# Optimization experiments

Measured on AMD Instinct MI355X. Metric: run time of the kernel, lower is better.

Reference implementation:

```python
import jax, jax.numpy as jnp
import numpy as np
from jax import lax

T, H, W = 2048, 128, 160


def setup_inputs() -> dict:
    key = jax.random.key(0)
    k1, = jax.random.split(key, 1)
    batch_x = jax.random.uniform(k1, (T, 1, H, W), dtype=jnp.float32)
    # params = [close, open, dhot] / 255 (defaults 1, 5, 8)
    params = jnp.array([1.0, 5.0, 8.0], dtype=jnp.float32) / 255.0
    HT0 = jnp.zeros((H, W), dtype=jnp.float32)
    LT0 = jnp.zeros((H, W), dtype=jnp.float32)
    # ConvTranspose2d(1,1,3,padding=1) with constant weight ones/(3**2/2) = 2/9;
    # symmetric kernel + padding=1 transposed conv == SAME-padded standard conv.
    kernel = jnp.full((1, 1, 3, 3), 2.0 / 9.0, dtype=jnp.float32)
    return {"batch_x": batch_x, "params": params, "HT0": HT0, "LT0": LT0, "kernel": kernel}


def reference(batch_x, params, HT0, LT0, kernel):
    d_close, d_open, d_hot = params[0], params[1], params[2]

    def step(carry, x):
        HT, LT = carry
        img = x[0]  # (H, W)
        # hot scores computed against *pre-update* thresholds
        tmpH_hot = jax.nn.sigmoid((img - HT - d_hot) * 500.0)
        tmpH = (img - HT) > 0
        HT = jnp.where(tmpH, HT + d_open, HT - d_close)
        tmpL_hot = jax.nn.sigmoid((LT - img - d_hot) * 500.0)
        tmpL = (LT - img) > 0
        LT = jnp.where(tmpL, LT - d_open, LT + d_close)
        return (HT, LT), tmpH_hot + tmpL_hot

    _, hot = lax.scan(step, (HT0, LT0), batch_x)  # hot: (T, H, W)

    # DiffErosion: relu(1 - conv(1 - x)) with SAME padding, batched over frames
    where_zero = (1.0 - hot)[:, None, :, :]  # (T, 1, H, W)
    sub = lax.conv_general_dilated(
        where_zero, kernel, window_strides=(1, 1), padding="SAME",
        dimension_numbers=("NCHW", "OIHW", "NCHW"))
    return jax.nn.relu(1.0 - sub)  # (T, 1, H, W)
```

## Files before the change

kernel.cpp:

```cpp
#include <hip/hip_runtime.h>


#define TILE_W 16
#define TILE_H 16
#define IN_W 14
#define IN_H 14
#define BUF 16
#define PRE 32

constexpr int T_FRAMES = 2048;
constexpr int H_IMG = 128;
constexpr int W_IMG = 160;
constexpr int HW = H_IMG * W_IMG;
constexpr float C1 = 721.3475204444817f;

constexpr size_t ws_needed(int snap) {
    return (size_t)(T_FRAMES / snap - 1) * HW * sizeof(float2);
}

__device__ __forceinline__ float dpp_from_left(float v) {
    return __int_as_float(__builtin_amdgcn_update_dpp(0, __float_as_int(v), 0x111, 0xF, 0xF, true));
}
__device__ __forceinline__ float dpp_from_right(float v) {
    return __int_as_float(__builtin_amdgcn_update_dpp(0, __float_as_int(v), 0x101, 0xF, 0xF, true));
}

template <int SNAP_>
__global__ __launch_bounds__(256, 1)
void svs_scan(const float* __restrict__ x, const float* __restrict__ params,
              const float* __restrict__ HT0, const float* __restrict__ LT0,
              float2* __restrict__ snap)
{
    constexpr int TEFF_ = T_FRAMES - SNAP_;
    const int pix = (int)blockIdx.x * 256 + (int)threadIdx.x;
    const float dC = params[0];
    const float dO = params[1];

    float HT = HT0[pix];
    float LT = LT0[pix];
    const float* xp = x + pix;

    float va[PRE], vb[PRE];
    #pragma unroll
    for (int i = 0; i < PRE; ++i) va[i] = xp[i * HW];
    __builtin_amdgcn_sched_barrier(0);

    for (int t = 0; t < TEFF_; t += 2 * PRE) {
        #pragma unroll
        for (int i = 0; i < PRE; ++i) vb[i] = xp[(t + PRE + i) * HW];
        __builtin_amdgcn_sched_barrier(0);
        #pragma unroll
        for (int i = 0; i < PRE; ++i) {
            const float img = va[i];
            HT = ((img - HT) > 0.0f) ? (HT + dO) : (HT - dC);
            LT = ((LT - img) > 0.0f) ? (LT - dO) : (LT + dC);
        }
        if (((t + PRE) % SNAP_) == 0) {
            const int k = (t + PRE) / SNAP_ - 1;
            if (k >= 0 && k < T_FRAMES / SNAP_ - 1)
                snap[(size_t)k * HW + pix] = make_float2(HT, LT);
        }
        if (t + 2 * PRE < TEFF_) {
            #pragma unroll
            for (int i = 0; i < PRE; ++i) va[i] = xp[(t + 2 * PRE + i) * HW];
        }
        __builtin_amdgcn_sched_barrier(0);
        #pragma unroll
        for (int i = 0; i < PRE; ++i) {
            const float img = vb[i];
            HT = ((img - HT) > 0.0f) ? (HT + dO) : (HT - dC);
            LT = ((LT - img) > 0.0f) ? (LT - dO) : (LT + dC);
        }
        if (((t + 2 * PRE) % SNAP_) == 0) {
            const int k = (t + 2 * PRE) / SNAP_ - 1;
            if (k < T_FRAMES / SNAP_ - 1)
                snap[(size_t)k * HW + pix] = make_float2(HT, LT);
        }
    }
}

template <int SNAP_>
__global__ __launch_bounds__(256)
void svs_compute(const float* __restrict__ x, const float* __restrict__ params,
                 const float* __restrict__ HT0, const float* __restrict__ LT0,
                 const float* __restrict__ kern, const float2* __restrict__ snap,
                 float* __restrict__ out)
{
    constexpr int TOTAL_ = 120 * (T_FRAMES / SNAP_);
    const int lin = (int)blockIdx.x + 12 * (int)blockIdx.y + 120 * (int)blockIdx.z;
    const int w   = (lin & 7) * (TOTAL_ / 8) + (lin >> 3);
    const int bx  = w % 12;
    const int by  = (w / 12) % 10;
    const int slice = w / 120;

    const int tx = threadIdx.x & 15;
    const int ty = threadIdx.x >> 4;
    const int gx = bx * IN_W + tx - 1;
    const int gy = by * IN_H + ty - 1;
    const int t0 = slice * SNAP_;

    const bool valid = (gx >= 0) & (gx < W_IMG) & (gy >= 0) & (gy < H_IMG);
    const int cx = min(max(gx, 0), W_IMG - 1);
    const int cy = min(max(gy, 0), H_IMG - 1);
    const int pix = cy * W_IMG + cx;

    const float dC   = params[0];
    const float dO   = params[1];
    const float dHot = params[2];
    const float kw   = kern[4];
    const float c0   = dHot * C1;

    float HT, LT;
    if (slice == 0) {
        HT = valid ? HT0[pix] : 0.0f;
        LT = valid ? LT0[pix] : 0.0f;
    } else {
        const float2 s = snap[(size_t)(slice - 1) * HW + pix];
        HT = valid ? s.x : 0.0f;
        LT = valid ? s.y : 0.0f;
    }

    __shared__ float sm[TILE_H][BUF][TILE_W + 1];

    const bool doOut = (tx >= 1) & (tx <= IN_W) & (ty >= 1) & (ty <= IN_H) & valid;
    const int ym = max(ty - 1, 0);
    const int yp = min(ty + 1, TILE_H - 1);
    const float* xp = x + pix;
    float* op = out + pix;

    float v[BUF], vn[BUF], hot[BUF];
    #pragma unroll
    for (int i = 0; i < BUF; ++i) v[i] = xp[(t0 + i) * HW];

    for (int tb = t0; tb < t0 + SNAP_; tb += BUF) {
        const bool more = (tb + BUF) < (t0 + SNAP_);
        if (more) {
            #pragma unroll
            for (int i = 0; i < BUF; ++i) vn[i] = xp[(tb + BUF + i) * HW];
        }
        __builtin_amdgcn_sched_barrier(0);
        #pragma unroll
        for (int i = 0; i < BUF; ++i) {
            const float img = v[i];
            const float aH = img - HT;
            const float eH = __builtin_amdgcn_exp2f(fmaf(aH, -C1, c0));
            const float hH = __builtin_amdgcn_rcpf(1.0f + eH);
            HT = (aH > 0.0f) ? (HT + dO) : (HT - dC);
            const float aL = LT - img;
            const float eL = __builtin_amdgcn_exp2f(fmaf(aL, -C1, c0));
            const float hL = __builtin_amdgcn_rcpf(1.0f + eL);
            LT = (aL > 0.0f) ? (LT - dO) : (LT + dC);
            hot[i] = valid ? (hH + hL) : 1.0f;
            sm[ty][i][tx] = hot[i];
        }
        __syncthreads();
        #pragma unroll
        for (int i = 0; i < BUF; ++i) {
            const float r0 = sm[ym][i][tx];
            const float r1 = sm[yp][i][tx];
            const float vs = r0 + hot[i] + r1;
            const float S  = vs + dpp_from_left(vs) + dpp_from_right(vs);
            float o = fmaf(S, kw, -1.0f);
            o = fmaxf(o, 0.0f);
            if (doOut) op[(tb + i) * HW] = o;
        }
        __syncthreads();
        if (more) {
            #pragma unroll
            for (int i = 0; i < BUF; ++i) v[i] = vn[i];
        }
    }
}

extern "C" void kernel_launch(void* const* d_in, const int* in_sizes, int n_in,
                              void* d_out, int out_size, void* d_ws, size_t ws_size,
                              hipStream_t stream) {
    const float* x      = (const float*)d_in[0];
    const float* params = (const float*)d_in[1];
    const float* HT0p   = (const float*)d_in[2];
    const float* LT0p   = (const float*)d_in[3];
    const float* kern   = (const float*)d_in[4];
    float* out = (float*)d_out;

    if (ws_size >= ws_needed(64)) {
        float2* snap = (float2*)d_ws;
        svs_scan<64><<<dim3(HW / 256), dim3(256), 0, stream>>>(x, params, HT0p, LT0p, snap);
        svs_compute<64><<<dim3(12, 10, T_FRAMES / 64), dim3(256), 0, stream>>>(
            x, params, HT0p, LT0p, kern, snap, out);
    } else if (ws_size >= ws_needed(128)) {
        float2* snap = (float2*)d_ws;
        svs_scan<128><<<dim3(HW / 256), dim3(256), 0, stream>>>(x, params, HT0p, LT0p, snap);
        svs_compute<128><<<dim3(12, 10, T_FRAMES / 128), dim3(256), 0, stream>>>(
            x, params, HT0p, LT0p, kern, snap, out);
    } else {
        svs_compute<2048><<<dim3(12, 10, 1), dim3(256), 0, stream>>>(
            x, params, HT0p, LT0p, kern, (const float2*)d_ws, out);
    }
}
```

Baseline: 168.3 us.

## Retile compute kernel to 32x8 output tiles with split halo/output threads

Replaces the 16x16 tile (14x14 outputs with DPP horizontal sums) with a 34x10 haloed tile computed by 340 threads, while 256 threads read the 3x3 window from shared memory to produce a 32x8 output tile with full-width coalesced stores. This cuts the redundant halo recomputation of the sigmoid scan and makes stores 32-wide and aligned. In exchange it drops the register double-buffered prefetch of x, halves BUF to 8, removes the block-index swizzle, and leaves 44 threads idle.

```diff
diff --git a/kernel.cpp b/kernel.cpp
--- a/kernel.cpp
+++ b/kernel.cpp
@@ -1,11 +1,7 @@
 #include <hip/hip_runtime.h>
 
 
-#define TILE_W 16
-#define TILE_H 16
-#define IN_W 14
-#define IN_H 14
-#define BUF 16
+#define BUF 8
 #define PRE 32
 
 constexpr int T_FRAMES = 2048;
@@ -16,13 +12,6 @@
 
 constexpr size_t ws_needed(int snap) {
     return (size_t)(T_FRAMES / snap - 1) * HW * sizeof(float2);
-}
-
-__device__ __forceinline__ float dpp_from_left(float v) {
-    return __int_as_float(__builtin_amdgcn_update_dpp(0, __float_as_int(v), 0x111, 0xF, 0xF, true));
-}
-__device__ __forceinline__ float dpp_from_right(float v) {
-    return __int_as_float(__builtin_amdgcn_update_dpp(0, __float_as_int(v), 0x101, 0xF, 0xF, true));
 }
 
 template <int SNAP_>
@@ -80,29 +69,17 @@
 }
 
 template <int SNAP_>
-__global__ __launch_bounds__(256)
-void svs_compute(const float* __restrict__ x, const float* __restrict__ params,
-                 const float* __restrict__ HT0, const float* __restrict__ LT0,
-                 const float* __restrict__ kern, const float2* __restrict__ snap,
-                 float* __restrict__ out)
+__global__ __launch_bounds__(384)
+void svs_compute2(const float* __restrict__ x, const float* __restrict__ params,
+                  const float* __restrict__ HT0, const float* __restrict__ LT0,
+                  const float* __restrict__ kern, const float2* __restrict__ snap,
+                  float* __restrict__ out)
 {
-    constexpr int TOTAL_ = 120 * (T_FRAMES / SNAP_);
-    const int lin = (int)blockIdx.x + 12 * (int)blockIdx.y + 120 * (int)blockIdx.z;
-    const int w   = (lin & 7) * (TOTAL_ / 8) + (lin >> 3);
-    const int bx  = w % 12;
-    const int by  = (w / 12) % 10;
-    const int slice = w / 120;
-
-    const int tx = threadIdx.x & 15;
-    const int ty = threadIdx.x >> 4;
-    const int gx = bx * IN_W + tx - 1;
-    const int gy = by * IN_H + ty - 1;
+    const int tc = (int)blockIdx.x;
+    const int tr = (int)blockIdx.y;
+    const int slice = (int)blockIdx.z;
     const int t0 = slice * SNAP_;
-
-    const bool valid = (gx >= 0) & (gx < W_IMG) & (gy >= 0) & (gy < H_IMG);
-    const int cx = min(max(gx, 0), W_IMG - 1);
-    const int cy = min(max(gy, 0), H_IMG - 1);
-    const int pix = cy * W_IMG + cx;
+    const int t = (int)threadIdx.x;
 
     const float dC   = params[0];
     const float dO   = params[1];
@@ -110,65 +87,70 @@
     const float kw   = kern[4];
     const float c0   = dHot * C1;
 
-    float HT, LT;
-    if (slice == 0) {
-        HT = valid ? HT0[pix] : 0.0f;
-        LT = valid ? LT0[pix] : 0.0f;
-    } else {
-        const float2 s = snap[(size_t)(slice - 1) * HW + pix];
-        HT = valid ? s.x : 0.0f;
-        LT = valid ? s.y : 0.0f;
+    const bool tA = (t < 340);
+    const int  ca = tA ? (t % 34) : 0;
+    const int  lr = tA ? (t / 34) : 0;
+    const int  gcol = tc * 32 + ca - 1;
+    const int  grow = tr * 8 + lr - 1;
+    const bool valid = tA & (gcol >= 0) & (gcol < W_IMG) & (grow >= 0) & (grow < H_IMG);
+    const int  pix = min(max(grow, 0), H_IMG - 1) * W_IMG + min(max(gcol, 0), W_IMG - 1);
+    const float* xp = x + pix;
+
+    float HT = 0.0f, LT = 0.0f;
+    if (tA) {
+        if (slice == 0) {
+            HT = valid ? HT0[pix] : 0.0f;
+            LT = valid ? LT0[pix] : 0.0f;
+        } else {
+            const float2 s = snap[(size_t)(slice - 1) * HW + pix];
+            HT = valid ? s.x : 0.0f;
+            LT = valid ? s.y : 0.0f;
+        }
     }
 
-    __shared__ float sm[TILE_H][BUF][TILE_W + 1];
+    const bool tB = (t < 256);
+    const int  oc = t & 31;
+    const int  orow = t >> 5;
+    float* op = out + (size_t)(tr * 8 + orow) * W_IMG + (tc * 32 + oc);
 
-    const bool doOut = (tx >= 1) & (tx <= IN_W) & (ty >= 1) & (ty <= IN_H) & valid;
-    const int ym = max(ty - 1, 0);
-    const int yp = min(ty + 1, TILE_H - 1);
-    const float* xp = x + pix;
-    float* op = out + pix;
-
-    float v[BUF], vn[BUF], hot[BUF];
-    #pragma unroll
-    for (int i = 0; i < BUF; ++i) v[i] = xp[(t0 + i) * HW];
+    __shared__ float sm[10][BUF][36];
 
     for (int tb = t0; tb < t0 + SNAP_; tb += BUF) {
-        const bool more = (tb + BUF) < (t0 + SNAP_);
-        if (more) {
+        float v[BUF];
+        if (tA) {
             #pragma unroll
-            for (int i = 0; i < BUF; ++i) vn[i] = xp[(tb + BUF + i) * HW];
+            for (int i = 0; i < BUF; ++i) v[i] = xp[(tb + i) * HW];
         }
         __builtin_amdgcn_sched_barrier(0);
-        #pragma unroll
-        for (int i = 0; i < BUF; ++i) {
-            const float img = v[i];
-            const float aH = img - HT;
-            const float eH = __builtin_amdgcn_exp2f(fmaf(aH, -C1, c0));
-            const float hH = __builtin_amdgcn_rcpf(1.0f + eH);
-            HT = (aH > 0.0f) ? (HT + dO) : (HT - dC);
-            const float aL = LT - img;
-            const float eL = __builtin_amdgcn_exp2f(fmaf(aL, -C1, c0));
-            const float hL = __builtin_amdgcn_rcpf(1.0f + eL);
-            LT = (aL > 0.0f) ? (LT - dO) : (LT + dC);
-            hot[i] = valid ? (hH + hL) : 1.0f;
-            sm[ty][i][tx] = hot[i];
+        if (tA) {
+            #pragma unroll
+            for (int i = 0; i < BUF; ++i) {
+                const float img = v[i];
+                const float aH = img - HT;
+                const float eH = __builtin_amdgcn_exp2f(fmaf(aH, -C1, c0));
+                const float hH = __builtin_amdgcn_rcpf(1.0f + eH);
+                HT = (aH > 0.0f) ? (HT + dO) : (HT - dC);
+                const float aL = LT - img;
+                const float eL = __builtin_amdgcn_exp2f(fmaf(aL, -C1, c0));
+                const float hL = __builtin_amdgcn_rcpf(1.0f + eL);
+                LT = (aL > 0.0f) ? (LT - dO) : (LT + dC);
+                sm[lr][i][ca] = valid ? (hH + hL) : 1.0f;
+            }
         }
         __syncthreads();
-        #pragma unroll
-        for (int i = 0; i < BUF; ++i) {
-            const float r0 = sm[ym][i][tx];
-            const float r1 = sm[yp][i][tx];
-            const float vs = r0 + hot[i] + r1;
-            const float S  = vs + dpp_from_left(vs) + dpp_from_right(vs);
-            float o = fmaf(S, kw, -1.0f);
-            o = fmaxf(o, 0.0f);
-            if (doOut) op[(tb + i) * HW] = o;
+        if (tB) {
+            #pragma unroll
+            for (int i = 0; i < BUF; ++i) {
+                const float cs0 = sm[orow][i][oc    ] + sm[orow + 1][i][oc    ] + sm[orow + 2][i][oc    ];
+                const float cs1 = sm[orow][i][oc + 1] + sm[orow + 1][i][oc + 1] + sm[orow + 2][i][oc + 1];
+                const float cs2 = sm[orow][i][oc + 2] + sm[orow + 1][i][oc + 2] + sm[orow + 2][i][oc + 2];
+                const float S = cs0 + cs1 + cs2;
+                float o = fmaf(S, kw, -1.0f);
+                o = fmaxf(o, 0.0f);
+                op[(size_t)(tb + i) * HW] = o;
+            }
         }
         __syncthreads();
-        if (more) {
-            #pragma unroll
-            for (int i = 0; i < BUF; ++i) v[i] = vn[i];
-        }
     }
 }
 
@@ -185,15 +167,15 @@
     if (ws_size >= ws_needed(64)) {
         float2* snap = (float2*)d_ws;
         svs_scan<64><<<dim3(HW / 256), dim3(256), 0, stream>>>(x, params, HT0p, LT0p, snap);
-        svs_compute<64><<<dim3(12, 10, T_FRAMES / 64), dim3(256), 0, stream>>>(
+        svs_compute2<64><<<dim3(5, 16, T_FRAMES / 64), dim3(384), 0, stream>>>(
             x, params, HT0p, LT0p, kern, snap, out);
     } else if (ws_size >= ws_needed(128)) {
         float2* snap = (float2*)d_ws;
         svs_scan<128><<<dim3(HW / 256), dim3(256), 0, stream>>>(x, params, HT0p, LT0p, snap);
-        svs_compute<128><<<dim3(12, 10, T_FRAMES / 128), dim3(256), 0, stream>>>(
+        svs_compute2<128><<<dim3(5, 16, T_FRAMES / 128), dim3(384), 0, stream>>>(
             x, params, HT0p, LT0p, kern, snap, out);
     } else {
-        svs_compute<2048><<<dim3(12, 10, 1), dim3(256), 0, stream>>>(
+        svs_compute2<2048><<<dim3(5, 16, 1), dim3(384), 0, stream>>>(
             x, params, HT0p, LT0p, kern, (const float2*)d_ws, out);
     }
 }
```

Measured after the change: 170.7 us. About the same (+1.4%).

## Stream scan inputs through a deep LDS ring via global_load_lds

Applied to the files above, without the earlier changes.

Replaces the register-double-buffered scan with a single-wave-per-block kernel that keeps a 63-deep ring of frames in LDS. Loads are issued asynchronously with global_load_lds and throttled by explicit vmcnt waits. Each serial step issues one new load, so many loads stay in flight per lane and memory latency is hidden without large register arrays. It also removes the register prefetch from the compute kernel. The risks are 64-thread blocks giving lower occupancy per CU and per-frame waitcnt overhead on the serial recurrence; the old scan is kept only for the smaller-workspace path.

```diff
diff --git a/kernel.cpp b/kernel.cpp
--- a/kernel.cpp
+++ b/kernel.cpp
@@ -7,6 +7,7 @@
 #define IN_H 14
 #define BUF 16
 #define PRE 32
+#define DEPTH 63
 
 constexpr int T_FRAMES = 2048;
 constexpr int H_IMG = 128;
@@ -25,14 +26,26 @@
     return __int_as_float(__builtin_amdgcn_update_dpp(0, __float_as_int(v), 0x101, 0xF, 0xF, true));
 }
 
+#define WAITCNT_VM(N) __builtin_amdgcn_s_waitcnt((((N) & 0xF) | (((N) >> 4) << 14) | (0x7 << 4) | (0xF << 8)))
+#define SB0() __builtin_amdgcn_sched_barrier(0)
+
+typedef const unsigned int __attribute__((address_space(1)))* gas_ptr;
+typedef unsigned int __attribute__((address_space(3)))* las_ptr;
+#define GLLDS(g, l)                                                          \
+    __builtin_amdgcn_global_load_lds(                                        \
+        (gas_ptr)(unsigned long long)(g),                                    \
+        (las_ptr)(unsigned)(unsigned long long)(l), 4, 0, 0)
+
 template <int SNAP_>
-__global__ __launch_bounds__(256, 1)
-void svs_scan(const float* __restrict__ x, const float* __restrict__ params,
-              const float* __restrict__ HT0, const float* __restrict__ LT0,
-              float2* __restrict__ snap)
+__global__ __launch_bounds__(64, 1)
+void svs_scan_lds(const float* __restrict__ x, const float* __restrict__ params,
+                  const float* __restrict__ HT0, const float* __restrict__ LT0,
+                  float2* __restrict__ snap)
 {
     constexpr int TEFF_ = T_FRAMES - SNAP_;
-    const int pix = (int)blockIdx.x * 256 + (int)threadIdx.x;
+    constexpr int NSNAP_ = T_FRAMES / SNAP_ - 1;
+    const int lane = (int)threadIdx.x;
+    const int pix  = (int)blockIdx.x * 64 + lane;
     const float dC = params[0];
     const float dO = params[1];
 
@@ -40,42 +53,39 @@
     float LT = LT0[pix];
     const float* xp = x + pix;
 
-    float va[PRE], vb[PRE];
-    #pragma unroll
-    for (int i = 0; i < PRE; ++i) va[i] = xp[i * HW];
-    __builtin_amdgcn_sched_barrier(0);
-
-    for (int t = 0; t < TEFF_; t += 2 * PRE) {
-        #pragma unroll
-        for (int i = 0; i < PRE; ++i) vb[i] = xp[(t + PRE + i) * HW];
-        __builtin_amdgcn_sched_barrier(0);
-        #pragma unroll
-        for (int i = 0; i < PRE; ++i) {
-            const float img = va[i];
-            HT = ((img - HT) > 0.0f) ? (HT + dO) : (HT - dC);
-            LT = ((LT - img) > 0.0f) ? (LT - dO) : (LT + dC);
-        }
-        if (((t + PRE) % SNAP_) == 0) {
-            const int k = (t + PRE) / SNAP_ - 1;
-            if (k >= 0 && k < T_FRAMES / SNAP_ - 1)
+    __shared__ float lds[DEPTH * 64];
+
+    #pragma unroll 1
+    for (int d = 0; d < DEPTH; ++d)
+        GLLDS(xp + (size_t)d * HW, &lds[d * 64]);
+
+    WAITCNT_VM(DEPTH - 1);
+    SB0();
+    float img_next = lds[lane];
+
+    int wslot = 0;
+    int rslot = 1;
+
+    #pragma unroll 1
+    for (int f = 0; f < TEFF_; ++f) {
+        const float img = img_next;
+        if (f + 1 < TEFF_) {
+            WAITCNT_VM(DEPTH - 4);
+            SB0();
+            img_next = lds[rslot * 64 + lane];
+        }
+        HT = ((img - HT) > 0.0f) ? (HT + dO) : (HT - dC);
+        LT = ((LT - img) > 0.0f) ? (LT - dO) : (LT + dC);
+        SB0();
+        if (f + DEPTH < TEFF_)
+            GLLDS(xp + (size_t)(f + DEPTH) * HW, &lds[wslot * 64]);
+        if ((f & (SNAP_ - 1)) == (SNAP_ - 1)) {
+            const int k = f / SNAP_;
+            if (k < NSNAP_)
                 snap[(size_t)k * HW + pix] = make_float2(HT, LT);
         }
-        if (t + 2 * PRE < TEFF_) {
-            #pragma unroll
-            for (int i = 0; i < PRE; ++i) va[i] = xp[(t + 2 * PRE + i) * HW];
-        }
-        __builtin_amdgcn_sched_barrier(0);
-        #pragma unroll
-        for (int i = 0; i < PRE; ++i) {
-            const float img = vb[i];
-            HT = ((img - HT) > 0.0f) ? (HT + dO) : (HT - dC);
-            LT = ((LT - img) > 0.0f) ? (LT - dO) : (LT + dC);
-        }
-        if (((t + 2 * PRE) % SNAP_) == 0) {
-            const int k = (t + 2 * PRE) / SNAP_ - 1;
-            if (k < T_FRAMES / SNAP_ - 1)
-                snap[(size_t)k * HW + pix] = make_float2(HT, LT);
-        }
+        if (++wslot == DEPTH) wslot = 0;
+        if (++rslot == DEPTH) rslot = 0;
     }
 }
 
@@ -128,17 +138,10 @@
     const float* xp = x + pix;
     float* op = out + pix;
 
-    float v[BUF], vn[BUF], hot[BUF];
-    #pragma unroll
-    for (int i = 0; i < BUF; ++i) v[i] = xp[(t0 + i) * HW];
-
     for (int tb = t0; tb < t0 + SNAP_; tb += BUF) {
-        const bool more = (tb + BUF) < (t0 + SNAP_);
-        if (more) {
-            #pragma unroll
-            for (int i = 0; i < BUF; ++i) vn[i] = xp[(tb + BUF + i) * HW];
-        }
-        __builtin_amdgcn_sched_barrier(0);
+        float v[BUF], hot[BUF];
+        #pragma unroll
+        for (int i = 0; i < BUF; ++i) v[i] = xp[(tb + i) * HW];
         #pragma unroll
         for (int i = 0; i < BUF; ++i) {
             const float img = v[i];
@@ -165,9 +168,59 @@
             if (doOut) op[(tb + i) * HW] = o;
         }
         __syncthreads();
-        if (more) {
+    }
+}
+
+template <int SNAP_>
+__global__ __launch_bounds__(256, 1)
+void svs_scan(const float* __restrict__ x, const float* __restrict__ params,
+              const float* __restrict__ HT0, const float* __restrict__ LT0,
+              float2* __restrict__ snap)
+{
+    constexpr int TEFF_ = T_FRAMES - SNAP_;
+    const int pix = (int)blockIdx.x * 256 + (int)threadIdx.x;
+    const float dC = params[0];
+    const float dO = params[1];
+
+    float HT = HT0[pix];
+    float LT = LT0[pix];
+    const float* xp = x + pix;
+
+    float va[PRE], vb[PRE];
+    #pragma unroll
+    for (int i = 0; i < PRE; ++i) va[i] = xp[i * HW];
+    __builtin_amdgcn_sched_barrier(0);
+
+    for (int t = 0; t < TEFF_; t += 2 * PRE) {
+        #pragma unroll
+        for (int i = 0; i < PRE; ++i) vb[i] = xp[(t + PRE + i) * HW];
+        __builtin_amdgcn_sched_barrier(0);
+        #pragma unroll
+        for (int i = 0; i < PRE; ++i) {
+            const float img = va[i];
+            HT = ((img - HT) > 0.0f) ? (HT + dO) : (HT - dC);
+            LT = ((LT - img) > 0.0f) ? (LT - dO) : (LT + dC);
+        }
+        if (((t + PRE) % SNAP_) == 0) {
+            const int k = (t + PRE) / SNAP_ - 1;
+            if (k >= 0 && k < T_FRAMES / SNAP_ - 1)
+                snap[(size_t)k * HW + pix] = make_float2(HT, LT);
+        }
+        if (t + 2 * PRE < TEFF_) {
             #pragma unroll
-            for (int i = 0; i < BUF; ++i) v[i] = vn[i];
+            for (int i = 0; i < PRE; ++i) va[i] = xp[(t + 2 * PRE + i) * HW];
+        }
+        __builtin_amdgcn_sched_barrier(0);
+        #pragma unroll
+        for (int i = 0; i < PRE; ++i) {
+            const float img = vb[i];
+            HT = ((img - HT) > 0.0f) ? (HT + dO) : (HT - dC);
+            LT = ((LT - img) > 0.0f) ? (LT - dO) : (LT + dC);
+        }
+        if (((t + 2 * PRE) % SNAP_) == 0) {
+            const int k = (t + 2 * PRE) / SNAP_ - 1;
+            if (k < T_FRAMES / SNAP_ - 1)
+                snap[(size_t)k * HW + pix] = make_float2(HT, LT);
         }
     }
 }
@@ -184,7 +237,8 @@
 
     if (ws_size >= ws_needed(64)) {
         float2* snap = (float2*)d_ws;
-        svs_scan<64><<<dim3(HW / 256), dim3(256), 0, stream>>>(x, params, HT0p, LT0p, snap);
+        svs_scan_lds<64><<<dim3(HW / 64), dim3(64), 0, stream>>>(
+            x, params, HT0p, LT0p, snap);
         svs_compute<64><<<dim3(12, 10, T_FRAMES / 64), dim3(256), 0, stream>>>(
             x, params, HT0p, LT0p, kern, snap, out);
     } else if (ws_size >= ws_needed(128)) {
```

Result: slower. 261.1 us (+55.1%).
